# Kernel optimization log

Hardware: AMD Instinct MI355X
Metric: run time of the kernel (lower is better)

The kernel has to match this reference:

```python
import jax, jax.numpy as jnp
import numpy as np

N_NODES = 100000
N_EDGES = 1600000
N_GRAPHS = 1000
NODES_PER_GRAPH = N_NODES // N_GRAPHS
IN_DIM, HID_DIM, OUT_DIM = 32, 64, 32


def setup_inputs() -> dict:
    key = jax.random.key(0)
    k_x, k_src, k_dst, k_w1, k_w2 = jax.random.split(key, 5)
    x = jax.random.normal(k_x, (N_NODES, IN_DIM), dtype=jnp.float32)
    src = jax.random.randint(k_src, (N_EDGES,), 0, N_NODES, dtype=jnp.int32)
    dst = jax.random.randint(k_dst, (N_EDGES,), 0, N_NODES, dtype=jnp.int32)
    edge_index = jnp.stack([src, dst], axis=0)
    batch = (jnp.arange(N_NODES, dtype=jnp.int32) // NODES_PER_GRAPH)
    W1 = jax.random.normal(k_w1, (IN_DIM, HID_DIM), dtype=jnp.float32) / np.sqrt(IN_DIM)
    b1 = jnp.zeros((HID_DIM,), dtype=jnp.float32)
    W2 = jax.random.normal(k_w2, (HID_DIM, OUT_DIM), dtype=jnp.float32) / np.sqrt(HID_DIM)
    b2 = jnp.zeros((OUT_DIM,), dtype=jnp.float32)
    return {"x": x, "edge_index": edge_index, "batch": batch,
            "W1": W1, "b1": b1, "W2": W2, "b2": b2}


def _gcn_conv(x, W, b, src, dst, deg_inv_sqrt):
    # PyG GCNConv: out = D^{-1/2}(A+I)D^{-1/2} X W + b, deg includes self-loops
    h = x @ W  # [N, F]
    norm = deg_inv_sqrt[src] * deg_inv_sqrt[dst]  # [E]
    agg = jax.ops.segment_sum(h[src] * norm[:, None], dst, num_segments=N_NODES)
    # self-loop contribution: norm = deg^{-1/2} * deg^{-1/2} = 1/deg
    agg = agg + h * (deg_inv_sqrt * deg_inv_sqrt)[:, None]
    return agg + b


def reference(x, edge_index, batch, W1, b1, W2, b2):
    src, dst = edge_index[0], edge_index[1]
    # degree at target nodes, with self-loops
    deg = 1.0 + jax.ops.segment_sum(jnp.ones_like(dst, dtype=x.dtype), dst,
                                    num_segments=N_NODES)
    deg_inv_sqrt = jax.lax.rsqrt(deg)
    h = jax.nn.relu(_gcn_conv(x, W1, b1, src, dst, deg_inv_sqrt))
    h = _gcn_conv(h, W2, b2, src, dst, deg_inv_sqrt)
    # per-graph mean pooling (fused segment mean)
    sums = jax.ops.segment_sum(h, batch, num_segments=N_GRAPHS)
    counts = jax.ops.segment_sum(jnp.ones((h.shape[0],), dtype=h.dtype), batch,
                                 num_segments=N_GRAPHS)
    return sums / counts[:, None]
```

## Files before the change

### kernel.cpp

```cpp
#include <hip/hip_runtime.h>

#define IN_DIM 32
#define HID_DIM 64
#define OUT_DIM 32

#define MAXBUCK 1024
#define CAP 2560
#define EPB 8192

typedef unsigned int u32;
typedef unsigned short u16;
typedef unsigned long long u64;
typedef __attribute__((ext_vector_type(8))) short bf16x8;
typedef __attribute__((ext_vector_type(4))) float f32x4;

static __device__ __forceinline__ u32 bf16rne(float f) {
    u32 u = __float_as_uint(f);
    return (u + 0x7FFFu + ((u >> 16) & 1u)) >> 16;
}
static __device__ __forceinline__ float blo(u32 u) { return __uint_as_float(u << 16); }
static __device__ __forceinline__ float bhi(u32 u) { return __uint_as_float(u & 0xFFFF0000u); }

__global__ __launch_bounds__(1024) void k_bin(const int* __restrict__ src,
                                              const int* __restrict__ dst,
                                              int* __restrict__ cursor,
                                              int* __restrict__ binned,
                                              int E, int nbuck, int npg, u32 M) {
    __shared__ int lcnt[MAXBUCK];
    __shared__ int lbase[MAXBUCK];
    int t = threadIdx.x;
    if (t < MAXBUCK) lcnt[t] = 0;
    __syncthreads();
    int base = blockIdx.x * EPB;
    int dreg[8], breg[8];
#pragma unroll
    for (int k = 0; k < 8; k++) {
        int e = base + k * 1024 + t;
        dreg[k] = (e < E) ? dst[e] : -1;
    }
#pragma unroll
    for (int k = 0; k < 8; k++) {
        if (dreg[k] >= 0) {
            breg[k] = (int)(((u64)(u32)dreg[k] * M) >> 38);
            atomicAdd(&lcnt[breg[k]], 1);
        }
    }
    __syncthreads();
    if (t < nbuck) {
        int c = lcnt[t];
        if (c) lbase[t] = atomicAdd(&cursor[t], c);
        lcnt[t] = 0;
    }
    __syncthreads();
#pragma unroll
    for (int k = 0; k < 8; k++) {
        if (dreg[k] >= 0) {
            int bk = breg[k];
            int dl = dreg[k] - bk * npg;
            int loc = lbase[bk] + atomicAdd(&lcnt[bk], 1);
            if (loc < CAP)
                binned[bk * CAP + loc] = (dl << 17) | src[base + k * 1024 + t];
        }
    }
}

__global__ __launch_bounds__(256) void k_csr(const int* __restrict__ binned,
                                             const int* __restrict__ cursor,
                                             const float* __restrict__ x,
                                             int2* __restrict__ row,
                                             float* __restrict__ dis,
                                             u16* __restrict__ g,
                                             int* __restrict__ meta,
                                             int N, int npg) {
    __shared__ int sEdge[CAP];
    __shared__ int sH[4][128];
    __shared__ int sExcl[128];
    __shared__ int sCur[128];
    __shared__ float sdis[128];
    __shared__ int wsum[2];
    int b = blockIdx.x;
    int t = threadIdx.x;
    int wid = t >> 6;
    int s0 = b * CAP;
    int cnt = cursor[b];
    if (cnt > CAP) cnt = CAP;

    for (int k = t; k < 4 * 128; k += 256) ((int*)sH)[k] = 0;
    __syncthreads();

    for (int k = t; k < cnt; k += 256) {
        int p = binned[s0 + k];
        sEdge[k] = p;
        atomicAdd(&sH[wid][p >> 17], 1);
    }
    __syncthreads();

    if (t < 128) {
        int myv = sH[0][t] + sH[1][t] + sH[2][t] + sH[3][t];
        int lane = t & 63;
        int incl = myv;
#pragma unroll
        for (int o = 1; o < 64; o <<= 1) {
            int up = __shfl_up(incl, o);
            if (lane >= o) incl += up;
        }
        if (lane == 63) wsum[t >> 6] = incl;
        sExcl[t] = incl - myv;
        sCur[t] = 0;
        sH[0][t] = myv;
    }
    __syncthreads();
    if (t < 128) {
        int exclv = sExcl[t] + ((t >= 64) ? wsum[0] : 0);
        sExcl[t] = exclv;
        int myv = sH[0][t];
        float d = rsqrtf(1.0f + (float)myv);
        sdis[t] = d;
        int node = b * npg + t;
        if (t < npg && node < N) {
            row[node] = make_int2(s0 + exclv, s0 + exclv + myv);
            dis[node] = d;
        }
    }
    __syncthreads();

    for (int k = t; k < cnt; k += 256) {
        int p = sEdge[k];
        int dl = p >> 17;
        int pos = sExcl[dl] + atomicAdd(&sCur[dl], 1);
        meta[s0 + pos] = p & 0x1FFFF;
    }

    int nbLo = b * npg;
    int nn = N - nbLo;
    if (nn > npg) nn = npg;
    if (nn < 0) nn = 0;
    int halfE = nn * 16;
    const float* xb = x + (size_t)nbLo * 32;
    u32* gb = (u32*)(g + (size_t)nbLo * 32);
    for (int j = t; j < halfE; j += 256) {
        int e0 = j * 2;
        float dd = sdis[e0 >> 5];
        gb[j] = bf16rne(dd * xb[e0]) | (bf16rne(dd * xb[e0 + 1]) << 16);
    }
}

__global__ __launch_bounds__(256) void k_agg(const u16* __restrict__ g,
                                             const int* __restrict__ meta,
                                             const int2* __restrict__ row,
                                             const float* __restrict__ dis,
                                             u16* __restrict__ outf, int N) {
    int gid = blockIdx.x * 256 + threadIdx.x;
    int i = gid >> 5;
    if (i >= N) return;
    int l = threadIdx.x & 31;
    int grp = (l >> 2) & 7;
    int sub = l & 3;
    const uint4* gv = (const uint4*)g;

    float a0 = 0.f, a1 = 0.f, a2 = 0.f, a3 = 0.f;
    float a4 = 0.f, a5 = 0.f, a6 = 0.f, a7 = 0.f;
    int2 rw = row[i];
    int e = rw.x, end = rw.y;
    for (; e + 16 <= end; e += 16) {
        int s0 = meta[e + grp];
        int s1 = meta[e + 8 + grp];
        uint4 v0 = gv[s0 * 4 + sub];
        uint4 v1 = gv[s1 * 4 + sub];
        a0 += blo(v0.x); a1 += bhi(v0.x); a2 += blo(v0.y); a3 += bhi(v0.y);
        a4 += blo(v0.z); a5 += bhi(v0.z); a6 += blo(v0.w); a7 += bhi(v0.w);
        a0 += blo(v1.x); a1 += bhi(v1.x); a2 += blo(v1.y); a3 += bhi(v1.y);
        a4 += blo(v1.z); a5 += bhi(v1.z); a6 += blo(v1.w); a7 += bhi(v1.w);
    }
    if (e + grp < end) {
        uint4 v = gv[meta[e + grp] * 4 + sub];
        a0 += blo(v.x); a1 += bhi(v.x); a2 += blo(v.y); a3 += bhi(v.y);
        a4 += blo(v.z); a5 += bhi(v.z); a6 += blo(v.w); a7 += bhi(v.w);
    }
    if (e + 8 + grp < end) {
        uint4 v = gv[meta[e + 8 + grp] * 4 + sub];
        a0 += blo(v.x); a1 += bhi(v.x); a2 += blo(v.y); a3 += bhi(v.y);
        a4 += blo(v.z); a5 += bhi(v.z); a6 += blo(v.w); a7 += bhi(v.w);
    }
#pragma unroll
    for (int m = 4; m <= 16; m <<= 1) {
        a0 += __shfl_xor(a0, m); a1 += __shfl_xor(a1, m);
        a2 += __shfl_xor(a2, m); a3 += __shfl_xor(a3, m);
        a4 += __shfl_xor(a4, m); a5 += __shfl_xor(a5, m);
        a6 += __shfl_xor(a6, m); a7 += __shfl_xor(a7, m);
    }
    if (grp == 0) {
        uint4 sv = gv[i * 4 + sub];
        float d = dis[i];
        u32 o0 = bf16rne(d * (a0 + blo(sv.x))) | (bf16rne(d * (a1 + bhi(sv.x))) << 16);
        u32 o1 = bf16rne(d * (a2 + blo(sv.y))) | (bf16rne(d * (a3 + bhi(sv.y))) << 16);
        u32 o2 = bf16rne(d * (a4 + blo(sv.z))) | (bf16rne(d * (a5 + bhi(sv.z))) << 16);
        u32 o3 = bf16rne(d * (a6 + blo(sv.w))) | (bf16rne(d * (a7 + bhi(sv.w))) << 16);
        ((uint4*)outf)[i * 4 + sub] = make_uint4(o0, o1, o2, o3);
    }
}

__global__ __launch_bounds__(256) void k_mlp(const u16* __restrict__ aggX,
                                             const float* __restrict__ W1,
                                             const float* __restrict__ b1,
                                             const float* __restrict__ W2,
                                             const float* __restrict__ dis,
                                             u16* __restrict__ t2, int N) {
    __shared__ float sHls[4][16 * 65];
    int t = threadIdx.x;
    int w = t >> 6;
    int L = t & 63;
    int q = L >> 4;
    int col = L & 15;
    int base = blockIdx.x * 64 + w * 16;

    int arow = base + col;
    uint4 av = (arow < N) ? ((const uint4*)aggX)[(size_t)arow * 4 + q]
                          : make_uint4(0, 0, 0, 0);
    bf16x8 afrag = *(bf16x8*)&av;

    bf16x8 b1f[4];
#pragma unroll
    for (int nt = 0; nt < 4; nt++) {
#pragma unroll
        for (int jj = 0; jj < 8; jj++)
            b1f[nt][jj] = (short)bf16rne(W1[(q * 8 + jj) * HID_DIM + nt * 16 + col]);
    }
    bf16x8 b2f[2][2];
#pragma unroll
    for (int ks = 0; ks < 2; ks++)
#pragma unroll
        for (int nt = 0; nt < 2; nt++) {
#pragma unroll
            for (int jj = 0; jj < 8; jj++)
                b2f[ks][nt][jj] =
                    (short)bf16rne(W2[(ks * 32 + q * 8 + jj) * OUT_DIM + nt * 16 + col]);
        }

#pragma unroll
    for (int nt = 0; nt < 4; nt++) {
        float bias = b1[nt * 16 + col];
        f32x4 c = {bias, bias, bias, bias};
        c = __builtin_amdgcn_mfma_f32_16x16x32_bf16(afrag, b1f[nt], c, 0, 0, 0);
#pragma unroll
        for (int r = 0; r < 4; r++)
            sHls[w][(q * 4 + r) * 65 + nt * 16 + col] = fmaxf(c[r], 0.0f);
    }
    __syncthreads();

    bf16x8 a2[2];
#pragma unroll
    for (int ks = 0; ks < 2; ks++) {
#pragma unroll
        for (int jj = 0; jj < 8; jj++)
            a2[ks][jj] = (short)bf16rne(sHls[w][col * 65 + ks * 32 + q * 8 + jj]);
    }

    f32x4 C2[2];
#pragma unroll
    for (int nt = 0; nt < 2; nt++) {
        f32x4 c = {0.f, 0.f, 0.f, 0.f};
        c = __builtin_amdgcn_mfma_f32_16x16x32_bf16(a2[0], b2f[0][nt], c, 0, 0, 0);
        c = __builtin_amdgcn_mfma_f32_16x16x32_bf16(a2[1], b2f[1][nt], c, 0, 0, 0);
        C2[nt] = c;
    }

#pragma unroll
    for (int r = 0; r < 4; r++) {
        int node = base + q * 4 + r;
        if (node < N) {
            float dd = dis[node];
            t2[(size_t)node * 32 + col]      = (u16)bf16rne(dd * C2[0][r]);
            t2[(size_t)node * 32 + 16 + col] = (u16)bf16rne(dd * C2[1][r]);
        }
    }
}

__global__ __launch_bounds__(512) void k_pool2(const int* __restrict__ binned,
                                               const int* __restrict__ cursor,
                                               const u16* __restrict__ gB,
                                               const float* __restrict__ dis,
                                               const float* __restrict__ b2,
                                               float* __restrict__ out,
                                               int N, int npg, float inv_npg) {
    __shared__ float sdis[128];
    __shared__ float sacc[32];
    int b = blockIdx.x;
    int t = threadIdx.x;
    if (t < 128) {
        int node = b * npg + t;
        sdis[t] = (t < npg && node < N) ? dis[node] : 0.0f;
    }
    if (t < 32) sacc[t] = 0.0f;
    __syncthreads();

    int s0 = b * CAP;
    int cnt = cursor[b];
    if (cnt > CAP) cnt = CAP;
    int sub = t & 3;
    int et = t >> 2;
    const uint4* gv = (const uint4*)gB;

    float a0 = 0.f, a1 = 0.f, a2 = 0.f, a3 = 0.f;
    float a4 = 0.f, a5 = 0.f, a6 = 0.f, a7 = 0.f;
#pragma unroll 4
    for (int e = et; e < cnt; e += 128) {
        int p = binned[s0 + e];
        uint4 v = gv[(u32)(p & 0x1FFFF) * 4 + sub];
        float w = sdis[p >> 17];
        a0 = fmaf(w, blo(v.x), a0); a1 = fmaf(w, bhi(v.x), a1);
        a2 = fmaf(w, blo(v.y), a2); a3 = fmaf(w, bhi(v.y), a3);
        a4 = fmaf(w, blo(v.z), a4); a5 = fmaf(w, bhi(v.z), a5);
        a6 = fmaf(w, blo(v.w), a6); a7 = fmaf(w, bhi(v.w), a7);
    }
#pragma unroll
    for (int m = 4; m <= 32; m <<= 1) {
        a0 += __shfl_xor(a0, m); a1 += __shfl_xor(a1, m);
        a2 += __shfl_xor(a2, m); a3 += __shfl_xor(a3, m);
        a4 += __shfl_xor(a4, m); a5 += __shfl_xor(a5, m);
        a6 += __shfl_xor(a6, m); a7 += __shfl_xor(a7, m);
    }
    if ((t & 63) < 4) {
        atomicAdd(&sacc[sub * 8 + 0], a0);
        atomicAdd(&sacc[sub * 8 + 1], a1);
        atomicAdd(&sacc[sub * 8 + 2], a2);
        atomicAdd(&sacc[sub * 8 + 3], a3);
        atomicAdd(&sacc[sub * 8 + 4], a4);
        atomicAdd(&sacc[sub * 8 + 5], a5);
        atomicAdd(&sacc[sub * 8 + 6], a6);
        atomicAdd(&sacc[sub * 8 + 7], a7);
    }

    float accs = 0.0f;
    int elems = npg * 32;
    const u16* gbase = gB + (size_t)b * npg * 32;
    int nbLo = b * npg;
    for (int k = t; k < elems; k += 512) {
        int node = k >> 5;
        if (nbLo + node < N)
            accs = fmaf(sdis[node], __uint_as_float((u32)gbase[k] << 16), accs);
    }
    atomicAdd(&sacc[t & 31], accs);
    __syncthreads();

    if (t < 32)
        out[b * 32 + t] = fmaf(sacc[t], inv_npg, b2[t]);
}

extern "C" void kernel_launch(void* const* d_in, const int* in_sizes, int n_in,
                              void* d_out, int out_size, void* d_ws, size_t ws_size,
                              hipStream_t stream) {
    const float* x   = (const float*)d_in[0];
    const int* eidx  = (const int*)d_in[1];
    const float* W1  = (const float*)d_in[3];
    const float* b1  = (const float*)d_in[4];
    const float* W2  = (const float*)d_in[5];
    const float* b2  = (const float*)d_in[6];
    float* out       = (float*)d_out;

    const int N = in_sizes[0] / IN_DIM;
    const int E = in_sizes[1] / 2;
    const int G = out_size / OUT_DIM;
    const int npg = N / G;
    const int nbuck = G;
    const int* src = eidx;
    const int* dst = eidx + E;
    const u32 M = (u32)(((1ull << 38) + npg - 1) / (u64)npg);

    char* ws = (char*)d_ws;
    size_t off = 0;
    auto alloc = [&](size_t bytes) -> char* {
        char* p = ws + off;
        off = (off + bytes + 255) & ~(size_t)255;
        return p;
    };
    int*   cursor = (int*)alloc(MAXBUCK * sizeof(int));
    int2*  row    = (int2*)alloc((size_t)N * sizeof(int2));
    float* dis    = (float*)alloc((size_t)N * sizeof(float));
    int*   binned = (int*)alloc((size_t)nbuck * CAP * sizeof(int));
    int*   meta   = (int*)alloc((size_t)nbuck * CAP * sizeof(int));
    u16*   g      = (u16*)alloc((size_t)N * IN_DIM * sizeof(u16));
    u16*   bufA   = (u16*)alloc((size_t)N * IN_DIM * sizeof(u16));
    u16*   bufB   = (u16*)alloc((size_t)N * OUT_DIM * sizeof(u16));
    (void)ws_size;

    hipMemsetAsync(cursor, 0, MAXBUCK * sizeof(int), stream);

    k_bin<<<(E + EPB - 1) / EPB, 1024, 0, stream>>>(src, dst, cursor, binned,
                                                    E, nbuck, npg, M);
    k_csr<<<nbuck, 256, 0, stream>>>(binned, cursor, x, row, dis, g, meta, N, npg);
    k_agg<<<((size_t)N * 32 + 255) / 256, 256, 0, stream>>>(g, meta, row, dis, bufA, N);
    k_mlp<<<(N + 63) / 64, 256, 0, stream>>>(bufA, W1, b1, W2, dis, bufB, N);
    k_pool2<<<nbuck, 512, 0, stream>>>(binned, cursor, bufB, dis, b2, out,
                                       N, npg, 1.0f / (float)npg);
}
```

Baseline: 159.4 us.

## Split edge binning into two-level radix partition with padded cursors

Replaces the single-pass edge binning (1000 buckets per block, global atomics on contiguous cursors) with a two-pass partition. Edges first go into 8 coarse regions, then each region is split into its 125 graph buckets with block-local histograms. Cursors are padded to a 16-int stride to avoid atomic contention on shared cache lines. The aim is fewer scattered writes and less atomic pressure, at the cost of an extra kernel launch and an extra pass through an intermediate buffer.

Measured after the change: 164.1 us. +3.0%, slower.

```diff
diff --git a/kernel.cpp b/kernel.cpp
--- a/kernel.cpp
+++ b/kernel.cpp
@@ -7,6 +7,10 @@
 #define MAXBUCK 1024
 #define CAP 2560
 #define EPB 8192
+#define NR 8
+#define RCAP 212992
+#define CPR 26
+#define CSTRIDE 16
 
 typedef unsigned int u32;
 typedef unsigned short u16;
@@ -21,18 +25,18 @@
 static __device__ __forceinline__ float blo(u32 u) { return __uint_as_float(u << 16); }
 static __device__ __forceinline__ float bhi(u32 u) { return __uint_as_float(u & 0xFFFF0000u); }
 
-__global__ __launch_bounds__(1024) void k_bin(const int* __restrict__ src,
-                                              const int* __restrict__ dst,
-                                              int* __restrict__ cursor,
-                                              int* __restrict__ binned,
-                                              int E, int nbuck, int npg, u32 M) {
-    __shared__ int lcnt[MAXBUCK];
-    __shared__ int lbase[MAXBUCK];
+__global__ __launch_bounds__(1024) void k_part(const int* __restrict__ src,
+                                               const int* __restrict__ dst,
+                                               int* __restrict__ rcur,
+                                               int* __restrict__ rbuf,
+                                               int E, int rspan, u32 M3) {
+    __shared__ int c8[NR];
+    __shared__ int b8[NR];
     int t = threadIdx.x;
-    if (t < MAXBUCK) lcnt[t] = 0;
+    if (t < NR) c8[t] = 0;
     __syncthreads();
     int base = blockIdx.x * EPB;
-    int dreg[8], breg[8];
+    int dreg[8], rreg[8];
 #pragma unroll
     for (int k = 0; k < 8; k++) {
         int e = base + k * 1024 + t;
@@ -41,25 +45,80 @@
 #pragma unroll
     for (int k = 0; k < 8; k++) {
         if (dreg[k] >= 0) {
-            breg[k] = (int)(((u64)(u32)dreg[k] * M) >> 38);
-            atomicAdd(&lcnt[breg[k]], 1);
-        }
-    }
-    __syncthreads();
-    if (t < nbuck) {
+            rreg[k] = (int)(((u64)(u32)dreg[k] * M3) >> 38);
+            atomicAdd(&c8[rreg[k]], 1);
+        }
+    }
+    __syncthreads();
+    if (t < NR) {
+        int c = c8[t];
+        b8[t] = c ? atomicAdd(&rcur[t], c) : 0;
+        c8[t] = 0;
+    }
+    __syncthreads();
+#pragma unroll
+    for (int k = 0; k < 8; k++) {
+        if (dreg[k] >= 0) {
+            int r = rreg[k];
+            int dlr = dreg[k] - r * rspan;
+            int loc = b8[r] + atomicAdd(&c8[r], 1);
+            if (loc < RCAP)
+                rbuf[(size_t)r * RCAP + loc] = (dlr << 17) | src[base + k * 1024 + t];
+        }
+    }
+}
+
+__global__ __launch_bounds__(1024) void k_bin2(const int* __restrict__ rbuf,
+                                               const int* __restrict__ rcur,
+                                               int* __restrict__ cursor,
+                                               int* __restrict__ binned,
+                                               int RW, int npg, int G, u32 M) {
+    __shared__ int lcnt[128];
+    __shared__ int lbase[128];
+    int rr = blockIdx.x / CPR;
+    int ck = blockIdx.x % CPR;
+    int t = threadIdx.x;
+    int n_r = rcur[rr];
+    if (n_r > RCAP) n_r = RCAP;
+    int base = ck * EPB;
+    if (base >= n_r) return;
+    int cnt = n_r - base;
+    if (cnt > EPB) cnt = EPB;
+    if (t < 128) lcnt[t] = 0;
+    __syncthreads();
+    const int* rb = rbuf + (size_t)rr * RCAP + base;
+    int preg[8], wreg[8];
+#pragma unroll
+    for (int k = 0; k < 8; k++) {
+        int e = k * 1024 + t;
+        preg[k] = (e < cnt) ? rb[e] : -1;
+    }
+#pragma unroll
+    for (int k = 0; k < 8; k++) {
+        if (preg[k] >= 0) {
+            u32 dlr = ((u32)preg[k]) >> 17;
+            wreg[k] = (int)(((u64)dlr * M) >> 38);
+            atomicAdd(&lcnt[wreg[k]], 1);
+        }
+    }
+    __syncthreads();
+    int wbase = rr * RW;
+    if (t < RW && wbase + t < G) {
         int c = lcnt[t];
-        if (c) lbase[t] = atomicAdd(&cursor[t], c);
+        lbase[t] = c ? atomicAdd(&cursor[(wbase + t) * CSTRIDE], c) : 0;
         lcnt[t] = 0;
     }
     __syncthreads();
 #pragma unroll
     for (int k = 0; k < 8; k++) {
-        if (dreg[k] >= 0) {
-            int bk = breg[k];
-            int dl = dreg[k] - bk * npg;
-            int loc = lbase[bk] + atomicAdd(&lcnt[bk], 1);
+        if (preg[k] >= 0) {
+            int wl = wreg[k];
+            int dlr = (int)(((u32)preg[k]) >> 17);
+            int dl = dlr - wl * npg;
+            int loc = lbase[wl] + atomicAdd(&lcnt[wl], 1);
             if (loc < CAP)
-                binned[bk * CAP + loc] = (dl << 17) | src[base + k * 1024 + t];
+                binned[(size_t)(wbase + wl) * CAP + loc] =
+                    (dl << 17) | (preg[k] & 0x1FFFF);
         }
     }
 }
@@ -82,7 +141,7 @@
     int t = threadIdx.x;
     int wid = t >> 6;
     int s0 = b * CAP;
-    int cnt = cursor[b];
+    int cnt = cursor[b * CSTRIDE];
     if (cnt > CAP) cnt = CAP;
 
     for (int k = t; k < 4 * 128; k += 256) ((int*)sH)[k] = 0;
@@ -295,7 +354,7 @@
     __syncthreads();
 
     int s0 = b * CAP;
-    int cnt = cursor[b];
+    int cnt = cursor[b * CSTRIDE];
     if (cnt > CAP) cnt = CAP;
     int sub = t & 3;
     int et = t >> 2;
@@ -363,9 +422,12 @@
     const int G = out_size / OUT_DIM;
     const int npg = N / G;
     const int nbuck = G;
+    const int RW = (G + NR - 1) / NR;
+    const int rspan = RW * npg;
     const int* src = eidx;
     const int* dst = eidx + E;
-    const u32 M = (u32)(((1ull << 38) + npg - 1) / (u64)npg);
+    const u32 M  = (u32)(((1ull << 38) + npg - 1) / (u64)npg);
+    const u32 M3 = (u32)(((1ull << 38) + rspan - 1) / (u64)rspan);
 
     char* ws = (char*)d_ws;
     size_t off = 0;
@@ -374,9 +436,11 @@
         off = (off + bytes + 255) & ~(size_t)255;
         return p;
     };
-    int*   cursor = (int*)alloc(MAXBUCK * sizeof(int));
+    int*   cursor = (int*)alloc((MAXBUCK * CSTRIDE + 16) * sizeof(int));
+    int*   rcur   = cursor + MAXBUCK * CSTRIDE;
     int2*  row    = (int2*)alloc((size_t)N * sizeof(int2));
     float* dis    = (float*)alloc((size_t)N * sizeof(float));
+    int*   rbuf   = (int*)alloc((size_t)NR * RCAP * sizeof(int));
     int*   binned = (int*)alloc((size_t)nbuck * CAP * sizeof(int));
     int*   meta   = (int*)alloc((size_t)nbuck * CAP * sizeof(int));
     u16*   g      = (u16*)alloc((size_t)N * IN_DIM * sizeof(u16));
@@ -384,10 +448,12 @@
     u16*   bufB   = (u16*)alloc((size_t)N * OUT_DIM * sizeof(u16));
     (void)ws_size;
 
-    hipMemsetAsync(cursor, 0, MAXBUCK * sizeof(int), stream);
-
-    k_bin<<<(E + EPB - 1) / EPB, 1024, 0, stream>>>(src, dst, cursor, binned,
-                                                    E, nbuck, npg, M);
+    hipMemsetAsync(cursor, 0, (MAXBUCK * CSTRIDE + 16) * sizeof(int), stream);
+
+    k_part<<<(E + EPB - 1) / EPB, 1024, 0, stream>>>(src, dst, rcur, rbuf,
+                                                     E, rspan, M3);
+    k_bin2<<<NR * CPR, 1024, 0, stream>>>(rbuf, rcur, cursor, binned,
+                                          RW, npg, G, M);
     k_csr<<<nbuck, 256, 0, stream>>>(binned, cursor, x, row, dis, g, meta, N, npg);
     k_agg<<<((size_t)N * 32 + 255) / 256, 256, 0, stream>>>(g, meta, row, dis, bufA, N);
     k_mlp<<<(N + 63) / 64, 256, 0, stream>>>(bufA, W1, b1, W2, dis, bufB, N);
```

## Fuse aggregation into MLP kernel via shared memory and pad bucket cursors

Applied to the files above, without the earlier changes.

Merges the first-layer edge aggregation kernel into the MLP kernel. Each block aggregates 64 nodes into a shared-memory tile, then runs the MFMA MLP directly on it, which removes the bufA global round trip and one launch. Separately, the per-bucket atomic cursors are spread out with a stride of 16 ints so they sit on separate cache lines, reducing atomic contention. The trade-off is that each fused block now does 8 sequential aggregation iterations per wavegroup, with fewer blocks in flight to hide gather latency, and it carries larger shared memory usage.

Result: slower. 181.6 us (+13.9%).

```diff
diff --git a/kernel.cpp b/kernel.cpp
--- a/kernel.cpp
+++ b/kernel.cpp
@@ -7,6 +7,7 @@
 #define MAXBUCK 1024
 #define CAP 2560
 #define EPB 8192
+#define CSTRIDE 16
 
 typedef unsigned int u32;
 typedef unsigned short u16;
@@ -48,7 +49,7 @@
     __syncthreads();
     if (t < nbuck) {
         int c = lcnt[t];
-        if (c) lbase[t] = atomicAdd(&cursor[t], c);
+        if (c) lbase[t] = atomicAdd(&cursor[t * CSTRIDE], c);
         lcnt[t] = 0;
     }
     __syncthreads();
@@ -82,7 +83,7 @@
     int t = threadIdx.x;
     int wid = t >> 6;
     int s0 = b * CAP;
-    int cnt = cursor[b];
+    int cnt = cursor[b * CSTRIDE];
     if (cnt > CAP) cnt = CAP;
 
     for (int k = t; k < 4 * 128; k += 256) ((int*)sH)[k] = 0;
@@ -145,133 +146,139 @@
     }
 }
 
-__global__ __launch_bounds__(256) void k_agg(const u16* __restrict__ g,
-                                             const int* __restrict__ meta,
-                                             const int2* __restrict__ row,
-                                             const float* __restrict__ dis,
-                                             u16* __restrict__ outf, int N) {
-    int gid = blockIdx.x * 256 + threadIdx.x;
-    int i = gid >> 5;
-    if (i >= N) return;
-    int l = threadIdx.x & 31;
-    int grp = (l >> 2) & 7;
-    int sub = l & 3;
-    const uint4* gv = (const uint4*)g;
-
-    float a0 = 0.f, a1 = 0.f, a2 = 0.f, a3 = 0.f;
-    float a4 = 0.f, a5 = 0.f, a6 = 0.f, a7 = 0.f;
-    int2 rw = row[i];
-    int e = rw.x, end = rw.y;
-    for (; e + 16 <= end; e += 16) {
-        int s0 = meta[e + grp];
-        int s1 = meta[e + 8 + grp];
-        uint4 v0 = gv[s0 * 4 + sub];
-        uint4 v1 = gv[s1 * 4 + sub];
-        a0 += blo(v0.x); a1 += bhi(v0.x); a2 += blo(v0.y); a3 += bhi(v0.y);
-        a4 += blo(v0.z); a5 += bhi(v0.z); a6 += blo(v0.w); a7 += bhi(v0.w);
-        a0 += blo(v1.x); a1 += bhi(v1.x); a2 += blo(v1.y); a3 += bhi(v1.y);
-        a4 += blo(v1.z); a5 += bhi(v1.z); a6 += blo(v1.w); a7 += bhi(v1.w);
-    }
-    if (e + grp < end) {
-        uint4 v = gv[meta[e + grp] * 4 + sub];
-        a0 += blo(v.x); a1 += bhi(v.x); a2 += blo(v.y); a3 += bhi(v.y);
-        a4 += blo(v.z); a5 += bhi(v.z); a6 += blo(v.w); a7 += bhi(v.w);
-    }
-    if (e + 8 + grp < end) {
-        uint4 v = gv[meta[e + 8 + grp] * 4 + sub];
-        a0 += blo(v.x); a1 += bhi(v.x); a2 += blo(v.y); a3 += bhi(v.y);
-        a4 += blo(v.z); a5 += bhi(v.z); a6 += blo(v.w); a7 += bhi(v.w);
-    }
-#pragma unroll
-    for (int m = 4; m <= 16; m <<= 1) {
-        a0 += __shfl_xor(a0, m); a1 += __shfl_xor(a1, m);
-        a2 += __shfl_xor(a2, m); a3 += __shfl_xor(a3, m);
-        a4 += __shfl_xor(a4, m); a5 += __shfl_xor(a5, m);
-        a6 += __shfl_xor(a6, m); a7 += __shfl_xor(a7, m);
-    }
-    if (grp == 0) {
-        uint4 sv = gv[i * 4 + sub];
-        float d = dis[i];
-        u32 o0 = bf16rne(d * (a0 + blo(sv.x))) | (bf16rne(d * (a1 + bhi(sv.x))) << 16);
-        u32 o1 = bf16rne(d * (a2 + blo(sv.y))) | (bf16rne(d * (a3 + bhi(sv.y))) << 16);
-        u32 o2 = bf16rne(d * (a4 + blo(sv.z))) | (bf16rne(d * (a5 + bhi(sv.z))) << 16);
-        u32 o3 = bf16rne(d * (a6 + blo(sv.w))) | (bf16rne(d * (a7 + bhi(sv.w))) << 16);
-        ((uint4*)outf)[i * 4 + sub] = make_uint4(o0, o1, o2, o3);
-    }
-}
-
-__global__ __launch_bounds__(256) void k_mlp(const u16* __restrict__ aggX,
-                                             const float* __restrict__ W1,
-                                             const float* __restrict__ b1,
-                                             const float* __restrict__ W2,
-                                             const float* __restrict__ dis,
-                                             u16* __restrict__ t2, int N) {
+__global__ __launch_bounds__(256) void k_aggmlp(const u16* __restrict__ g,
+                                                const int* __restrict__ meta,
+                                                const int2* __restrict__ row,
+                                                const float* __restrict__ dis,
+                                                const float* __restrict__ W1,
+                                                const float* __restrict__ b1,
+                                                const float* __restrict__ W2,
+                                                u16* __restrict__ t2, int N) {
+    __shared__ u32 sAgg[64][16];
     __shared__ float sHls[4][16 * 65];
     int t = threadIdx.x;
-    int w = t >> 6;
-    int L = t & 63;
-    int q = L >> 4;
-    int col = L & 15;
-    int base = blockIdx.x * 64 + w * 16;
-
-    int arow = base + col;
-    uint4 av = (arow < N) ? ((const uint4*)aggX)[(size_t)arow * 4 + q]
-                          : make_uint4(0, 0, 0, 0);
-    bf16x8 afrag = *(bf16x8*)&av;
-
-    bf16x8 b1f[4];
-#pragma unroll
-    for (int nt = 0; nt < 4; nt++) {
-#pragma unroll
-        for (int jj = 0; jj < 8; jj++)
-            b1f[nt][jj] = (short)bf16rne(W1[(q * 8 + jj) * HID_DIM + nt * 16 + col]);
-    }
-    bf16x8 b2f[2][2];
-#pragma unroll
-    for (int ks = 0; ks < 2; ks++)
+    int blk = blockIdx.x;
+    int nodeBase = blk * 64;
+
+    {
+        int grpIdx = t >> 5;
+        int l = t & 31;
+        int grp = (l >> 2) & 7;
+        int sub = l & 3;
+        const uint4* gv = (const uint4*)g;
+#pragma unroll
+        for (int it = 0; it < 8; it++) {
+            int i = nodeBase + it * 8 + grpIdx;
+            if (i < N) {
+                float a0 = 0.f, a1 = 0.f, a2 = 0.f, a3 = 0.f;
+                float a4 = 0.f, a5 = 0.f, a6 = 0.f, a7 = 0.f;
+                int2 rw = row[i];
+                int e = rw.x, end = rw.y;
+                for (; e + 16 <= end; e += 16) {
+                    int s0e = meta[e + grp];
+                    int s1e = meta[e + 8 + grp];
+                    uint4 v0 = gv[s0e * 4 + sub];
+                    uint4 v1 = gv[s1e * 4 + sub];
+                    a0 += blo(v0.x); a1 += bhi(v0.x); a2 += blo(v0.y); a3 += bhi(v0.y);
+                    a4 += blo(v0.z); a5 += bhi(v0.z); a6 += blo(v0.w); a7 += bhi(v0.w);
+                    a0 += blo(v1.x); a1 += bhi(v1.x); a2 += blo(v1.y); a3 += bhi(v1.y);
+                    a4 += blo(v1.z); a5 += bhi(v1.z); a6 += blo(v1.w); a7 += bhi(v1.w);
+                }
+                if (e + grp < end) {
+                    uint4 v = gv[meta[e + grp] * 4 + sub];
+                    a0 += blo(v.x); a1 += bhi(v.x); a2 += blo(v.y); a3 += bhi(v.y);
+                    a4 += blo(v.z); a5 += bhi(v.z); a6 += blo(v.w); a7 += bhi(v.w);
+                }
+                if (e + 8 + grp < end) {
+                    uint4 v = gv[meta[e + 8 + grp] * 4 + sub];
+                    a0 += blo(v.x); a1 += bhi(v.x); a2 += blo(v.y); a3 += bhi(v.y);
+                    a4 += blo(v.z); a5 += bhi(v.z); a6 += blo(v.w); a7 += bhi(v.w);
+                }
+#pragma unroll
+                for (int m = 4; m <= 16; m <<= 1) {
+                    a0 += __shfl_xor(a0, m); a1 += __shfl_xor(a1, m);
+                    a2 += __shfl_xor(a2, m); a3 += __shfl_xor(a3, m);
+                    a4 += __shfl_xor(a4, m); a5 += __shfl_xor(a5, m);
+                    a6 += __shfl_xor(a6, m); a7 += __shfl_xor(a7, m);
+                }
+                if (grp == 0) {
+                    uint4 sv = gv[i * 4 + sub];
+                    float d = dis[i];
+                    u32 o0 = bf16rne(d * (a0 + blo(sv.x))) | (bf16rne(d * (a1 + bhi(sv.x))) << 16);
+                    u32 o1 = bf16rne(d * (a2 + blo(sv.y))) | (bf16rne(d * (a3 + bhi(sv.y))) << 16);
+                    u32 o2 = bf16rne(d * (a4 + blo(sv.z))) | (bf16rne(d * (a5 + bhi(sv.z))) << 16);
+                    u32 o3 = bf16rne(d * (a6 + blo(sv.w))) | (bf16rne(d * (a7 + bhi(sv.w))) << 16);
+                    ((uint4*)sAgg)[(it * 8 + grpIdx) * 4 + sub] = make_uint4(o0, o1, o2, o3);
+                }
+            }
+        }
+    }
+    __syncthreads();
+
+    {
+        int w = t >> 6;
+        int L = t & 63;
+        int q = L >> 4;
+        int col = L & 15;
+        int base = nodeBase + w * 16;
+
+        bf16x8 b1f[4];
+#pragma unroll
+        for (int nt = 0; nt < 4; nt++) {
+#pragma unroll
+            for (int jj = 0; jj < 8; jj++)
+                b1f[nt][jj] = (short)bf16rne(W1[(q * 8 + jj) * HID_DIM + nt * 16 + col]);
+        }
+        bf16x8 b2f[2][2];
+#pragma unroll
+        for (int ks = 0; ks < 2; ks++)
+#pragma unroll
+            for (int nt = 0; nt < 2; nt++) {
+#pragma unroll
+                for (int jj = 0; jj < 8; jj++)
+                    b2f[ks][nt][jj] =
+                        (short)bf16rne(W2[(ks * 32 + q * 8 + jj) * OUT_DIM + nt * 16 + col]);
+            }
+
+        uint4 av = ((const uint4*)sAgg)[(w * 16 + col) * 4 + q];
+        bf16x8 afrag = *(bf16x8*)&av;
+
+#pragma unroll
+        for (int nt = 0; nt < 4; nt++) {
+            float bias = b1[nt * 16 + col];
+            f32x4 c = {bias, bias, bias, bias};
+            c = __builtin_amdgcn_mfma_f32_16x16x32_bf16(afrag, b1f[nt], c, 0, 0, 0);
+#pragma unroll
+            for (int r = 0; r < 4; r++)
+                sHls[w][(q * 4 + r) * 65 + nt * 16 + col] = fmaxf(c[r], 0.0f);
+        }
+        __syncthreads();
+
+        bf16x8 a2[2];
+#pragma unroll
+        for (int ks = 0; ks < 2; ks++) {
+#pragma unroll
+            for (int jj = 0; jj < 8; jj++)
+                a2[ks][jj] = (short)bf16rne(sHls[w][col * 65 + ks * 32 + q * 8 + jj]);
+        }
+
+        f32x4 C2[2];
 #pragma unroll
         for (int nt = 0; nt < 2; nt++) {
-#pragma unroll
-            for (int jj = 0; jj < 8; jj++)
-                b2f[ks][nt][jj] =
-                    (short)bf16rne(W2[(ks * 32 + q * 8 + jj) * OUT_DIM + nt * 16 + col]);
-        }
-
-#pragma unroll
-    for (int nt = 0; nt < 4; nt++) {
-        float bias = b1[nt * 16 + col];
-        f32x4 c = {bias, bias, bias, bias};
-        c = __builtin_amdgcn_mfma_f32_16x16x32_bf16(afrag, b1f[nt], c, 0, 0, 0);
-#pragma unroll
-        for (int r = 0; r < 4; r++)
-            sHls[w][(q * 4 + r) * 65 + nt * 16 + col] = fmaxf(c[r], 0.0f);
-    }
-    __syncthreads();
-
-    bf16x8 a2[2];
-#pragma unroll
-    for (int ks = 0; ks < 2; ks++) {
-#pragma unroll
-        for (int jj = 0; jj < 8; jj++)
-            a2[ks][jj] = (short)bf16rne(sHls[w][col * 65 + ks * 32 + q * 8 + jj]);
-    }
-
-    f32x4 C2[2];
-#pragma unroll
-    for (int nt = 0; nt < 2; nt++) {
-        f32x4 c = {0.f, 0.f, 0.f, 0.f};
-        c = __builtin_amdgcn_mfma_f32_16x16x32_bf16(a2[0], b2f[0][nt], c, 0, 0, 0);
-        c = __builtin_amdgcn_mfma_f32_16x16x32_bf16(a2[1], b2f[1][nt], c, 0, 0, 0);
-        C2[nt] = c;
-    }
-
-#pragma unroll
-    for (int r = 0; r < 4; r++) {
-        int node = base + q * 4 + r;
-        if (node < N) {
-            float dd = dis[node];
-            t2[(size_t)node * 32 + col]      = (u16)bf16rne(dd * C2[0][r]);
-            t2[(size_t)node * 32 + 16 + col] = (u16)bf16rne(dd * C2[1][r]);
+            f32x4 c = {0.f, 0.f, 0.f, 0.f};
+            c = __builtin_amdgcn_mfma_f32_16x16x32_bf16(a2[0], b2f[0][nt], c, 0, 0, 0);
+            c = __builtin_amdgcn_mfma_f32_16x16x32_bf16(a2[1], b2f[1][nt], c, 0, 0, 0);
+            C2[nt] = c;
+        }
+
+#pragma unroll
+        for (int r = 0; r < 4; r++) {
+            int node = base + q * 4 + r;
+            if (node < N) {
+                float dd = dis[node];
+                t2[(size_t)node * 32 + col]      = (u16)bf16rne(dd * C2[0][r]);
+                t2[(size_t)node * 32 + 16 + col] = (u16)bf16rne(dd * C2[1][r]);
+            }
         }
     }
 }
@@ -295,7 +302,7 @@
     __syncthreads();
 
     int s0 = b * CAP;
-    int cnt = cursor[b];
+    int cnt = cursor[b * CSTRIDE];
     if (cnt > CAP) cnt = CAP;
     int sub = t & 3;
     int et = t >> 2;
@@ -374,23 +381,22 @@
         off = (off + bytes + 255) & ~(size_t)255;
         return p;
     };
-    int*   cursor = (int*)alloc(MAXBUCK * sizeof(int));
+    int*   cursor = (int*)alloc((size_t)MAXBUCK * CSTRIDE * sizeof(int));
     int2*  row    = (int2*)alloc((size_t)N * sizeof(int2));
     float* dis    = (float*)alloc((size_t)N * sizeof(float));
     int*   binned = (int*)alloc((size_t)nbuck * CAP * sizeof(int));
     int*   meta   = (int*)alloc((size_t)nbuck * CAP * sizeof(int));
     u16*   g      = (u16*)alloc((size_t)N * IN_DIM * sizeof(u16));
-    u16*   bufA   = (u16*)alloc((size_t)N * IN_DIM * sizeof(u16));
     u16*   bufB   = (u16*)alloc((size_t)N * OUT_DIM * sizeof(u16));
     (void)ws_size;
 
-    hipMemsetAsync(cursor, 0, MAXBUCK * sizeof(int), stream);
+    hipMemsetAsync(cursor, 0, (size_t)MAXBUCK * CSTRIDE * sizeof(int), stream);
 
     k_bin<<<(E + EPB - 1) / EPB, 1024, 0, stream>>>(src, dst, cursor, binned,
                                                     E, nbuck, npg, M);
     k_csr<<<nbuck, 256, 0, stream>>>(binned, cursor, x, row, dis, g, meta, N, npg);
-    k_agg<<<((size_t)N * 32 + 255) / 256, 256, 0, stream>>>(g, meta, row, dis, bufA, N);
-    k_mlp<<<(N + 63) / 64, 256, 0, stream>>>(bufA, W1, b1, W2, dis, bufB, N);
+    k_aggmlp<<<(N + 63) / 64, 256, 0, stream>>>(g, meta, row, dis, W1, b1, W2,
+                                                bufB, N);
     k_pool2<<<nbuck, 512, 0, stream>>>(binned, cursor, bufB, dis, b2, out,
                                        N, npg, 1.0f / (float)npg);
 }
```

## Stage binned edges in LDS for coalesced scatter and pad global bucket cursors

Applied to the files above, without the earlier changes.

The binning kernel now computes a block-local prefix sum over bucket counts and sorts its 8192 edges by bucket in shared memory. It then writes them out in bucket-contiguous runs, so the global stores are mostly coalesced instead of scattered. Global bucket cursors are padded to a 64-byte stride to reduce atomic contention on shared cache lines. This costs about 60KB of LDS per block, which lowers occupancy, and adds extra barriers and a scan.

After: 161.6 us. Within noise of the previous version (+1.4%).

```diff
diff --git a/kernel.cpp b/kernel.cpp
--- a/kernel.cpp
+++ b/kernel.cpp
@@ -7,6 +7,7 @@
 #define MAXBUCK 1024
 #define CAP 2560
 #define EPB 8192
+#define CSTRIDE 16
 
 typedef unsigned int u32;
 typedef unsigned short u16;
@@ -26,11 +27,16 @@
                                               int* __restrict__ cursor,
                                               int* __restrict__ binned,
                                               int E, int nbuck, int npg, u32 M) {
-    __shared__ int lcnt[MAXBUCK];
+    __shared__ int sExcl[MAXBUCK];
+    __shared__ int sCur[MAXBUCK];
     __shared__ int lbase[MAXBUCK];
+    __shared__ int sEdge[EPB];
+    __shared__ u16 sWin[EPB];
+    __shared__ int wpart[16];
     int t = threadIdx.x;
-    if (t < MAXBUCK) lcnt[t] = 0;
-    __syncthreads();
+    sCur[t] = 0;
+    __syncthreads();
+
     int base = blockIdx.x * EPB;
     int dreg[8], breg[8];
 #pragma unroll
@@ -42,25 +48,56 @@
     for (int k = 0; k < 8; k++) {
         if (dreg[k] >= 0) {
             breg[k] = (int)(((u64)(u32)dreg[k] * M) >> 38);
-            atomicAdd(&lcnt[breg[k]], 1);
-        }
-    }
-    __syncthreads();
-    if (t < nbuck) {
-        int c = lcnt[t];
-        if (c) lbase[t] = atomicAdd(&cursor[t], c);
-        lcnt[t] = 0;
-    }
-    __syncthreads();
+            atomicAdd(&sCur[breg[k]], 1);
+        }
+    }
+    __syncthreads();
+
+    int v = sCur[t];
+    int lane = t & 63;
+    int incl = v;
+#pragma unroll
+    for (int o = 1; o < 64; o <<= 1) {
+        int u = __shfl_up(incl, o);
+        if (lane >= o) incl += u;
+    }
+    if (lane == 63) wpart[t >> 6] = incl;
+    __syncthreads();
+    if (t < 16) {
+        int p = wpart[t];
+#pragma unroll
+        for (int o = 1; o < 16; o <<= 1) {
+            int u = __shfl_up(p, o);
+            if (lane >= o) p += u;
+        }
+        wpart[t] = p;
+    }
+    __syncthreads();
+    int excl = incl - v + ((t >> 6) ? wpart[(t >> 6) - 1] : 0);
+    int tot = wpart[15];
+    __syncthreads();
+    sExcl[t] = excl;
+    sCur[t] = 0;
+    if (t < nbuck && v > 0)
+        lbase[t] = atomicAdd(&cursor[t * CSTRIDE], v);
+    __syncthreads();
+
 #pragma unroll
     for (int k = 0; k < 8; k++) {
         if (dreg[k] >= 0) {
-            int bk = breg[k];
-            int dl = dreg[k] - bk * npg;
-            int loc = lbase[bk] + atomicAdd(&lcnt[bk], 1);
-            if (loc < CAP)
-                binned[bk * CAP + loc] = (dl << 17) | src[base + k * 1024 + t];
-        }
+            int w = breg[k];
+            int dl = dreg[k] - w * npg;
+            int loc = sExcl[w] + atomicAdd(&sCur[w], 1);
+            sEdge[loc] = (dl << 17) | src[base + k * 1024 + t];
+            sWin[loc] = (u16)w;
+        }
+    }
+    __syncthreads();
+
+    for (int j = t; j < tot; j += 1024) {
+        int w = sWin[j];
+        int pos = lbase[w] + (j - sExcl[w]);
+        if (pos < CAP) binned[w * CAP + pos] = sEdge[j];
     }
 }
 
@@ -82,7 +119,7 @@
     int t = threadIdx.x;
     int wid = t >> 6;
     int s0 = b * CAP;
-    int cnt = cursor[b];
+    int cnt = cursor[b * CSTRIDE];
     if (cnt > CAP) cnt = CAP;
 
     for (int k = t; k < 4 * 128; k += 256) ((int*)sH)[k] = 0;
@@ -295,7 +332,7 @@
     __syncthreads();
 
     int s0 = b * CAP;
-    int cnt = cursor[b];
+    int cnt = cursor[b * CSTRIDE];
     if (cnt > CAP) cnt = CAP;
     int sub = t & 3;
     int et = t >> 2;
@@ -374,7 +411,7 @@
         off = (off + bytes + 255) & ~(size_t)255;
         return p;
     };
-    int*   cursor = (int*)alloc(MAXBUCK * sizeof(int));
+    int*   cursor = (int*)alloc((size_t)MAXBUCK * CSTRIDE * sizeof(int));
     int2*  row    = (int2*)alloc((size_t)N * sizeof(int2));
     float* dis    = (float*)alloc((size_t)N * sizeof(float));
     int*   binned = (int*)alloc((size_t)nbuck * CAP * sizeof(int));
@@ -384,7 +421,7 @@
     u16*   bufB   = (u16*)alloc((size_t)N * OUT_DIM * sizeof(u16));
     (void)ws_size;
 
-    hipMemsetAsync(cursor, 0, MAXBUCK * sizeof(int), stream);
+    hipMemsetAsync(cursor, 0, (size_t)MAXBUCK * CSTRIDE * sizeof(int), stream);
 
     k_bin<<<(E + EPB - 1) / EPB, 1024, 0, stream>>>(src, dst, cursor, binned,
                                                     E, nbuck, npg, M);
```
